# Performance work log

Measured on AMD Instinct MI355X. Metric: run time of the kernel, lower is better.

The kernel has to match this reference:

```python
import math
import jax, jax.numpy as jnp
import numpy as np

B, S, D, H = 8, 1024, 512, 8
DK = D // H
P = 2 * S - 1


def rel_shift(x):
    # x: [b, h, qlen, plen] -> [b, h, qlen, plen-1] (Transformer-XL shift)
    b, h, qL, pL = x.shape
    x = x.reshape(b, h, pL, qL)[:, :, 1:, :]
    return x.reshape(b, h, qL, pL - 1)


def setup_inputs() -> dict:
    key = jax.random.key(0)
    ks = jax.random.split(key, 16)
    glorot = lambda k, shp: (jax.random.uniform(k, shp, jnp.float32, -1.0, 1.0)
                             * np.sqrt(6.0 / (shp[0] + shp[1])))
    inp = {
        "q": jax.random.normal(ks[0], (B, S, D), jnp.float32),
        "k": jax.random.normal(ks[1], (B, S, D), jnp.float32),
        "v": jax.random.normal(ks[2], (B, S, D), jnp.float32),
        "pos_emb": jax.random.normal(ks[3], (1, P, D), jnp.float32),
        "mask": jax.random.randint(ks[4], (B, 1, S), 0, 2).astype(bool),
        "Wq": glorot(ks[5], (D, D)), "bq": jnp.zeros((D,), jnp.float32),
        "Wk": glorot(ks[6], (D, D)), "bk": jnp.zeros((D,), jnp.float32),
        "Wv": glorot(ks[7], (D, D)), "bv": jnp.zeros((D,), jnp.float32),
        "Wo": glorot(ks[8], (D, D)), "bo": jnp.zeros((D,), jnp.float32),
        "Wpos": glorot(ks[9], (D, D)),
        "pos_bias_u": glorot(ks[10], (H, DK)),
        "pos_bias_v": glorot(ks[11], (H, DK)),
    }
    return inp


def reference(q, k, v, pos_emb, mask, Wq, bq, Wk, bk, Wv, bv, Wo, bo,
              Wpos, pos_bias_u, pos_bias_v):
    b = q.shape[0]
    # projections -> [b, h, s, dk]
    qh = (q @ Wq.T + bq).reshape(b, -1, H, DK).transpose(0, 2, 1, 3)
    kh = (k @ Wk.T + bk).reshape(b, -1, H, DK).transpose(0, 2, 1, 3)
    vh = (v @ Wv.T + bv).reshape(b, -1, H, DK).transpose(0, 2, 1, 3)
    # positional projection -> [h, p, dk] (pos batch dim is 1)
    p = (pos_emb @ Wpos.T).reshape(pos_emb.shape[0], -1, H, DK).transpose(0, 2, 1, 3)[0]

    q_u = qh + pos_bias_u[None, :, None, :]
    q_v = qh + pos_bias_v[None, :, None, :]

    matrix_bd = jnp.einsum("bhsd,hpd->bhsp", q_v, p)
    matrix_bd = rel_shift(matrix_bd)
    matrix_ac = jnp.einsum("bhsd,bhtd->bhst", q_u, kh)
    matrix_bd = matrix_bd[:, :, :, : matrix_ac.shape[-1]]

    scores = (matrix_ac + matrix_bd) / math.sqrt(DK)
    # mask [b,1,s] -> [b,1,1,s] broadcast over heads and query dim
    scores = jnp.where(mask[:, None], -10000.0, scores)
    attn = jax.nn.softmax(scores, axis=-1)
    x = jnp.einsum("bhst,bhtd->bhsd", attn, vh)
    x = x.transpose(0, 2, 1, 3).reshape(b, -1, H * DK)
    return x @ Wo.T + bo
```

## Files before the change

### kernel.cpp

```cpp
#include <hip/hip_runtime.h>
#include <math.h>

#define S_LEN 1024
#define N_HEAD 8
#define P_LEN 2047
#define B_SZ 8
#define QT 32
#define KT 32

typedef __attribute__((ext_vector_type(8))) short bf16x8;
typedef __attribute__((ext_vector_type(4))) float f32x4;

union f4u { float4 v; float f[4]; };
union bfz { bf16x8 v; uint4 u; };

__device__ __forceinline__ unsigned short f2bf(float x) {
  unsigned b = __float_as_uint(x);
  b = b + 0x7FFF + ((b >> 16) & 1);
  return (unsigned short)(b >> 16);
}
__device__ __forceinline__ float bf2f(unsigned short h) {
  return __uint_as_float(((unsigned)h) << 16);
}

__global__ __launch_bounds__(256) void mask_prep(const void* __restrict__ mask,
                                                 int* __restrict__ mw) {
  const unsigned int* u = (const unsigned int*)mask;
  bool all01 = true, allf = true;
#pragma unroll
  for (int j = 0; j < 16; ++j) {
    unsigned int x = u[j];
    all01 &= (x <= 1u);
    allf &= (x == 0u || x == 0x3f800000u);
  }
  int i = blockIdx.x * 256 + threadIdx.x;
  int v;
  if (all01) v = (((const int*)mask)[i] != 0);
  else if (allf) v = (((const float*)mask)[i] != 0.0f);
  else v = (((const unsigned char*)mask)[i] != 0);
  mw[i] = v;
}

template<int MODE>
__global__ __launch_bounds__(256) void gemm512(
    const float* __restrict__ A, const float* __restrict__ W,
    const float* __restrict__ bias, const float* __restrict__ pbu,
    const float* __restrict__ pbv, float* __restrict__ fo,
    unsigned short* __restrict__ o1h, unsigned short* __restrict__ o1l,
    unsigned short* __restrict__ o2h, unsigned short* __restrict__ o2l,
    int M)
{
  __shared__ float As[64][36];
  __shared__ float Wt[32][68];
  const int tid = threadIdx.x;
  const int ty = tid >> 4, tx = tid & 15;
  const int m0 = blockIdx.x * 64, n0 = blockIdx.y * 64;
  const int lr = tid >> 3;
  const int lc = (tid & 7) << 2;
  float acc[4][4] = {};

  for (int k0 = 0; k0 < 512; k0 += 32) {
#pragma unroll
    for (int hh = 0; hh < 2; ++hh) {
      int r = lr + hh * 32;
      int gm = m0 + r;
      float4 av = make_float4(0.f, 0.f, 0.f, 0.f);
      if (gm < M) av = *(const float4*)(A + (size_t)gm * 512 + k0 + lc);
      *(float4*)&As[r][lc] = av;
      float4 wv = *(const float4*)(W + (size_t)(n0 + r) * 512 + k0 + lc);
      Wt[lc + 0][r] = wv.x;
      Wt[lc + 1][r] = wv.y;
      Wt[lc + 2][r] = wv.z;
      Wt[lc + 3][r] = wv.w;
    }
    __syncthreads();
#pragma unroll
    for (int kk = 0; kk < 32; kk += 4) {
      f4u a[4], w[4];
#pragma unroll
      for (int i = 0; i < 4; ++i) a[i].v = *(float4*)&As[ty * 4 + i][kk];
#pragma unroll
      for (int q = 0; q < 4; ++q) w[q].v = *(float4*)&Wt[kk + q][tx * 4];
#pragma unroll
      for (int i = 0; i < 4; ++i)
#pragma unroll
        for (int q = 0; q < 4; ++q)
#pragma unroll
          for (int j = 0; j < 4; ++j)
            acc[i][j] = fmaf(a[i].f[q], w[q].f[j], acc[i][j]);
    }
    __syncthreads();
  }

#pragma unroll
  for (int i = 0; i < 4; ++i) {
    int m = m0 + ty * 4 + i;
    if (MODE == 2 && m >= M) continue;
    int n = n0 + tx * 4;
    if constexpr (MODE == 3) {
      f4u r;
#pragma unroll
      for (int j = 0; j < 4; ++j) r.f[j] = acc[i][j] + bias[n + j];
      *(float4*)(fo + (size_t)m * 512 + n) = r.v;
    } else if constexpr (MODE == 2) {
      int hI = n >> 6, dk = n & 63;
      size_t idx = ((size_t)(hI * P_LEN + m) << 6) + dk;
      ushort4 hv, lv;
      unsigned short h;
      h = f2bf(acc[i][0]); hv.x = h; lv.x = f2bf(acc[i][0] - bf2f(h));
      h = f2bf(acc[i][1]); hv.y = h; lv.y = f2bf(acc[i][1] - bf2f(h));
      h = f2bf(acc[i][2]); hv.z = h; lv.z = f2bf(acc[i][2] - bf2f(h));
      h = f2bf(acc[i][3]); hv.w = h; lv.w = f2bf(acc[i][3] - bf2f(h));
      *(ushort4*)(o1h + idx) = hv;
      *(ushort4*)(o1l + idx) = lv;
    } else {
      int bI = m >> 10, s = m & 1023, hI = n >> 6, dk = n & 63;
      size_t idx = ((size_t)(((bI * 8 + hI) << 10) + s) << 6) + dk;
      float vb[4];
#pragma unroll
      for (int j = 0; j < 4; ++j) vb[j] = acc[i][j] + bias[n + j];
      if constexpr (MODE == 0) {
        ushort4 hv, lv;
        unsigned short h;
        h = f2bf(vb[0]); hv.x = h; lv.x = f2bf(vb[0] - bf2f(h));
        h = f2bf(vb[1]); hv.y = h; lv.y = f2bf(vb[1] - bf2f(h));
        h = f2bf(vb[2]); hv.z = h; lv.z = f2bf(vb[2] - bf2f(h));
        h = f2bf(vb[3]); hv.w = h; lv.w = f2bf(vb[3] - bf2f(h));
        *(ushort4*)(o1h + idx) = hv;
        *(ushort4*)(o1l + idx) = lv;
      } else {
        ushort4 hu, lu, hv2, lv2;
        unsigned short h;
        float t;
        t = vb[0] + pbu[n + 0]; h = f2bf(t); hu.x = h; lu.x = f2bf(t - bf2f(h));
        t = vb[1] + pbu[n + 1]; h = f2bf(t); hu.y = h; lu.y = f2bf(t - bf2f(h));
        t = vb[2] + pbu[n + 2]; h = f2bf(t); hu.z = h; lu.z = f2bf(t - bf2f(h));
        t = vb[3] + pbu[n + 3]; h = f2bf(t); hu.w = h; lu.w = f2bf(t - bf2f(h));
        t = vb[0] + pbv[n + 0]; h = f2bf(t); hv2.x = h; lv2.x = f2bf(t - bf2f(h));
        t = vb[1] + pbv[n + 1]; h = f2bf(t); hv2.y = h; lv2.y = f2bf(t - bf2f(h));
        t = vb[2] + pbv[n + 2]; h = f2bf(t); hv2.z = h; lv2.z = f2bf(t - bf2f(h));
        t = vb[3] + pbv[n + 3]; h = f2bf(t); hv2.w = h; lv2.w = f2bf(t - bf2f(h));
        *(ushort4*)(o1h + idx) = hu;  *(ushort4*)(o1l + idx) = lu;
        *(ushort4*)(o2h + idx) = hv2; *(ushort4*)(o2l + idx) = lv2;
      }
    }
  }
}

__global__ __launch_bounds__(256) void vtrans(
    const unsigned short* __restrict__ src_h, const unsigned short* __restrict__ src_l,
    unsigned short* __restrict__ dst_h, unsigned short* __restrict__ dst_l)
{
  __shared__ unsigned short tile[64 * 72];
  const int tid = threadIdx.x;
  const int bh = blockIdx.x >> 4, st = blockIdx.x & 15;
  const int s0 = st << 6;
  const int r = tid >> 2;
  const int c0 = (tid & 3) << 4;
  const size_t ibase = (((size_t)(bh << 10) + s0 + r) << 6) + c0;
  const size_t obase = ((size_t)(bh << 6)) << 10;
#pragma unroll
  for (int pl = 0; pl < 2; ++pl) {
    const unsigned short* src = pl ? src_l : src_h;
    unsigned short* dst = pl ? dst_l : dst_h;
    *(uint4*)&tile[r * 72 + c0] = *(const uint4*)(src + ibase);
    *(uint4*)&tile[r * 72 + c0 + 8] = *(const uint4*)(src + ibase + 8);
    __syncthreads();
    unsigned short buf[16] __attribute__((aligned(16)));
#pragma unroll
    for (int i = 0; i < 16; ++i) buf[i] = tile[(c0 + i) * 72 + r];
    *(uint4*)(dst + obase + ((size_t)r << 10) + s0 + c0) = *(uint4*)&buf[0];
    *(uint4*)(dst + obase + ((size_t)r << 10) + s0 + c0 + 8) = *(uint4*)&buf[8];
    __syncthreads();
  }
}

__global__ __launch_bounds__(256, 3) void attn_kernel(
    const unsigned short* __restrict__ quh, const unsigned short* __restrict__ qul,
    const unsigned short* __restrict__ qvh, const unsigned short* __restrict__ qvl,
    const unsigned short* __restrict__ khh, const unsigned short* __restrict__ khl,
    const unsigned short* __restrict__ vth, const unsigned short* __restrict__ vtl,
    const unsigned short* __restrict__ pph, const unsigned short* __restrict__ ppl,
    const int* __restrict__ mw, float* __restrict__ ctx)
{
  __shared__ float zs[32 * 68];
  __shared__ unsigned short ph_s[32 * 40], pl_s[32 * 40];
  __shared__ float red[2][32][2];

  const int tid = threadIdx.x;
  const int wid = tid >> 6, lane = tid & 63;
  const int g = lane >> 4, ln = lane & 15;
  const int rt = wid >> 1, ct = wid & 1;
  const int R0 = rt << 4, T0 = ct << 4;

  const int bid = blockIdx.x;
  const int xcd = bid & 7;
  const int i0 = bid >> 3;
  const int bh = (xcd << 3) + (i0 >> 5);
  const int s0 = (i0 & 31) * QT;
  const int b = bh >> 3, h = bh & 7;

  const size_t qbase = ((size_t)((bh << 10) + s0)) << 6;
  const size_t kbase = ((size_t)(bh << 10)) << 6;
  const size_t vtb = ((size_t)(bh << 6)) << 10;
  const size_t ppb = ((size_t)(h * P_LEN)) << 6;

  bf16x8 qa_h[2], qa_l[2], qb_h[2], qb_l[2];
  {
    const size_t qo = qbase + (((size_t)(R0 + ln)) << 6) + (g << 3);
#pragma unroll
    for (int dblk = 0; dblk < 2; ++dblk) {
      qa_h[dblk] = *(const bf16x8*)(quh + qo + dblk * 32);
      qa_l[dblk] = *(const bf16x8*)(qul + qo + dblk * 32);
      qb_h[dblk] = *(const bf16x8*)(qvh + qo + dblk * 32);
      qb_l[dblk] = *(const bf16x8*)(qvl + qo + dblk * 32);
    }
  }

  float wrapW = 0.f;
  if (s0 == 0) {
    const unsigned short* q1h = qvh + ((((size_t)(bh << 10)) + 1) << 6);
    const unsigned short* q1l = qvl + ((((size_t)(bh << 10)) + 1) << 6);
    for (int d = 0; d < 64; ++d)
      wrapW += (bf2f(q1h[d]) + bf2f(q1l[d])) * (bf2f(pph[ppb + d]) + bf2f(ppl[ppb + d]));
  }
  const bool wrapT = (s0 == 0) && (wid == 1) && (lane == 15);

  f32x4 oA[2] = {{0.f, 0.f, 0.f, 0.f}, {0.f, 0.f, 0.f, 0.f}};
  float m_run[4], l_run[4];
#pragma unroll
  for (int r = 0; r < 4; ++r) { m_run[r] = -1e30f; l_run[r] = 0.f; }

  for (int t0 = 0; t0 < S_LEN; t0 += KT) {
    f32x4 ac = {0.f, 0.f, 0.f, 0.f};
    {
      const size_t ko = kbase + (((size_t)(t0 + T0 + ln)) << 6) + (g << 3);
#pragma unroll
      for (int dblk = 0; dblk < 2; ++dblk) {
        bf16x8 kh_ = *(const bf16x8*)(khh + ko + dblk * 32);
        bf16x8 kl_ = *(const bf16x8*)(khl + ko + dblk * 32);
        ac = __builtin_amdgcn_mfma_f32_16x16x32_bf16(qa_l[dblk], kh_, ac, 0, 0, 0);
        ac = __builtin_amdgcn_mfma_f32_16x16x32_bf16(qa_h[dblk], kl_, ac, 0, 0, 0);
        ac = __builtin_amdgcn_mfma_f32_16x16x32_bf16(qa_h[dblk], kh_, ac, 0, 0, 0);
      }
    }
    const int pmin = 993 + t0 - s0;
#pragma unroll
    for (int ut = 0; ut < 2; ++ut) {
      const int U0 = (ct << 5) + (ut << 4);
      const int p = pmin + U0 + ln;
      f32x4 z = {0.f, 0.f, 0.f, 0.f};
      bfz bh_[2], bl_[2];
      if (p < P_LEN) {
        const size_t po = ppb + (((size_t)p) << 6) + (g << 3);
        bh_[0].v = *(const bf16x8*)(pph + po);
        bh_[1].v = *(const bf16x8*)(pph + po + 32);
        bl_[0].v = *(const bf16x8*)(ppl + po);
        bl_[1].v = *(const bf16x8*)(ppl + po + 32);
      } else {
        bh_[0].u = bh_[1].u = bl_[0].u = bl_[1].u = make_uint4(0, 0, 0, 0);
      }
#pragma unroll
      for (int dblk = 0; dblk < 2; ++dblk) {
        z = __builtin_amdgcn_mfma_f32_16x16x32_bf16(qb_l[dblk], bh_[dblk].v, z, 0, 0, 0);
        z = __builtin_amdgcn_mfma_f32_16x16x32_bf16(qb_h[dblk], bl_[dblk].v, z, 0, 0, 0);
        z = __builtin_amdgcn_mfma_f32_16x16x32_bf16(qb_h[dblk], bh_[dblk].v, z, 0, 0, 0);
      }
#pragma unroll
      for (int r = 0; r < 4; ++r)
        zs[(R0 + (g << 2) + r) * 68 + U0 + ln] = z[r];
    }
    __syncthreads();

    const int t = T0 + ln;
    const int mval = mw[(b << 10) + t0 + t];
    float sc[4], ml[4], sl[4];
#pragma unroll
    for (int r = 0; r < 4; ++r) {
      const int row = R0 + (g << 2) + r;
      float bdv = zs[row * 68 + (t - row + 31)];
      if (wrapT && r == 0 && t0 == S_LEN - KT) bdv = wrapW;
      float v = (ac[r] + bdv) * 0.125f;
      sc[r] = mval ? -10000.f : v;
    }
#pragma unroll
    for (int r = 0; r < 4; ++r) {
      float mx = sc[r];
#pragma unroll
      for (int off = 1; off < 16; off <<= 1) mx = fmaxf(mx, __shfl_xor(mx, off));
      ml[r] = mx;
      float e = __expf(sc[r] - mx);
      float s = e;
#pragma unroll
      for (int off = 1; off < 16; off <<= 1) s += __shfl_xor(s, off);
      sl[r] = s;
      sc[r] = e;
    }
    if (ln == 0) {
#pragma unroll
      for (int r = 0; r < 4; ++r) {
        red[ct][R0 + (g << 2) + r][0] = ml[r];
        red[ct][R0 + (g << 2) + r][1] = sl[r];
      }
    }
    __syncthreads();

#pragma unroll
    for (int r = 0; r < 4; ++r) {
      const int row = R0 + (g << 2) + r;
      const float mo = red[ct ^ 1][row][0];
      const float so = red[ct ^ 1][row][1];
      const float mn = fmaxf(m_run[r], fmaxf(ml[r], mo));
      const float corr = __expf(m_run[r] - mn);
      l_run[r] = l_run[r] * corr + sl[r] * __expf(ml[r] - mn) + so * __expf(mo - mn);
      m_run[r] = mn;
      oA[0][r] *= corr;
      oA[1][r] *= corr;
      const float p = sc[r] * __expf(ml[r] - mn);
      const unsigned short hp = f2bf(p);
      ph_s[row * 40 + t] = hp;
      pl_s[row * 40 + t] = f2bf(p - bf2f(hp));
    }
    __syncthreads();

    bf16x8 pa_h = *(const bf16x8*)&ph_s[(R0 + ln) * 40 + (g << 3)];
    bf16x8 pa_l = *(const bf16x8*)&pl_s[(R0 + ln) * 40 + (g << 3)];
#pragma unroll
    for (int dkt = 0; dkt < 2; ++dkt) {
      const int dk = (ct << 5) + (dkt << 4) + ln;
      const size_t vo = vtb + (((size_t)dk) << 10) + t0 + (g << 3);
      bf16x8 vh_ = *(const bf16x8*)(vth + vo);
      bf16x8 vl_ = *(const bf16x8*)(vtl + vo);
      oA[dkt] = __builtin_amdgcn_mfma_f32_16x16x32_bf16(pa_l, vh_, oA[dkt], 0, 0, 0);
      oA[dkt] = __builtin_amdgcn_mfma_f32_16x16x32_bf16(pa_h, vl_, oA[dkt], 0, 0, 0);
      oA[dkt] = __builtin_amdgcn_mfma_f32_16x16x32_bf16(pa_h, vh_, oA[dkt], 0, 0, 0);
    }
  }

#pragma unroll
  for (int r = 0; r < 4; ++r) {
    const float inv = 1.0f / l_run[r];
    const int s = s0 + R0 + (g << 2) + r;
    float* cp = ctx + (((size_t)((b << 10) + s)) << 9) + (h << 6);
    cp[(ct << 5) + ln] = oA[0][r] * inv;
    cp[(ct << 5) + 16 + ln] = oA[1][r] * inv;
  }
}

extern "C" void kernel_launch(void* const* d_in, const int* in_sizes, int n_in,
                              void* d_out, int out_size, void* d_ws, size_t ws_size,
                              hipStream_t stream) {
  const float* q    = (const float*)d_in[0];
  const float* k    = (const float*)d_in[1];
  const float* v    = (const float*)d_in[2];
  const float* pos  = (const float*)d_in[3];
  const void*  mask = d_in[4];
  const float* Wq   = (const float*)d_in[5];
  const float* bq   = (const float*)d_in[6];
  const float* Wk   = (const float*)d_in[7];
  const float* bk   = (const float*)d_in[8];
  const float* Wv   = (const float*)d_in[9];
  const float* bv   = (const float*)d_in[10];
  const float* Wo   = (const float*)d_in[11];
  const float* bo   = (const float*)d_in[12];
  const float* Wpos = (const float*)d_in[13];
  const float* pbu  = (const float*)d_in[14];
  const float* pbv  = (const float*)d_in[15];
  float* out = (float*)d_out;

  unsigned short* us = (unsigned short*)d_ws;
  const size_t SZ  = (size_t)B_SZ * N_HEAD * S_LEN * 64;
  const size_t SZP = (size_t)N_HEAD * P_LEN * 64;
  unsigned short* quh = us;
  unsigned short* qul = quh + SZ;
  unsigned short* qvh = qul + SZ;
  unsigned short* qvl = qvh + SZ;
  unsigned short* khh = qvl + SZ;
  unsigned short* khl = khh + SZ;
  unsigned short* vth = khl + SZ;
  unsigned short* vtl = vth + SZ;
  unsigned short* pph = vtl + SZ;
  unsigned short* ppl = pph + SZP;
  float* ctxW = (float*)(ppl + SZP);
  unsigned short* vhh = (unsigned short*)ctxW;
  unsigned short* vhl = vhh + SZ;
  int* mwW = (int*)(ctxW + SZ);

  mask_prep<<<dim3(B_SZ * S_LEN / 256), 256, 0, stream>>>(mask, mwW);

  gemm512<1><<<dim3(128, 8), 256, 0, stream>>>(q, Wq, bq, pbu, pbv, nullptr,
                                               quh, qul, qvh, qvl, 8192);
  gemm512<0><<<dim3(128, 8), 256, 0, stream>>>(k, Wk, bk, nullptr, nullptr, nullptr,
                                               khh, khl, nullptr, nullptr, 8192);
  gemm512<0><<<dim3(128, 8), 256, 0, stream>>>(v, Wv, bv, nullptr, nullptr, nullptr,
                                               vhh, vhl, nullptr, nullptr, 8192);
  gemm512<2><<<dim3(32, 8), 256, 0, stream>>>(pos, Wpos, nullptr, nullptr, nullptr, nullptr,
                                              pph, ppl, nullptr, nullptr, P_LEN);

  vtrans<<<dim3(64 * 16), 256, 0, stream>>>(vhh, vhl, vth, vtl);

  attn_kernel<<<dim3(2048), 256, 0, stream>>>(quh, qul, qvh, qvl, khh, khl,
                                              vth, vtl, pph, ppl, mwW, ctxW);

  gemm512<3><<<dim3(128, 8), 256, 0, stream>>>(ctxW, Wo, bo, nullptr, nullptr, out,
                                               nullptr, nullptr, nullptr, nullptr, 8192);
}
```

Baseline: 876.9 us.

## Software-pipeline K and positional tile loads with register double buffering

The attention loop is unrolled by two using macros, with register double buffers for K and positional-embedding fragments. The next tile's loads are issued before the current tile's MFMA and softmax work, and V loads are hoisted to the start of each iteration. This is meant to hide global-memory latency behind compute and barriers. The extra live registers lower the occupancy hint from 3 to 2 blocks per CU, which risks less latency hiding across waves.

```diff
diff --git a/kernel.cpp b/kernel.cpp
--- a/kernel.cpp
+++ b/kernel.cpp
@@ -175,7 +175,122 @@
   }
 }
 
-__global__ __launch_bounds__(256, 3) void attn_kernel(
+#define MFMA_B(a, b, c) __builtin_amdgcn_mfma_f32_16x16x32_bf16(a, b, c, 0, 0, 0)
+
+#define DECL_KB(S) \
+  bf16x8 S##kh0, S##kh1, S##kl0, S##kl1; \
+  bfz S##b0h0, S##b0h1, S##b0l0, S##b0l1, S##b1h0, S##b1h1, S##b1l0, S##b1l1;
+
+#define LOAD_KB(S, T0V) { \
+  const size_t ko_ = kbase + (((size_t)((T0V) + T0 + ln)) << 6) + (g << 3); \
+  S##kh0 = *(const bf16x8*)(khh + ko_); \
+  S##kh1 = *(const bf16x8*)(khh + ko_ + 32); \
+  S##kl0 = *(const bf16x8*)(khl + ko_); \
+  S##kl1 = *(const bf16x8*)(khl + ko_ + 32); \
+  const int pm_ = 993 + (T0V) - s0 + (ct << 5) + ln; \
+  if (pm_ < P_LEN) { \
+    const size_t po_ = ppb + (((size_t)pm_) << 6) + (g << 3); \
+    S##b0h0.v = *(const bf16x8*)(pph + po_); \
+    S##b0h1.v = *(const bf16x8*)(pph + po_ + 32); \
+    S##b0l0.v = *(const bf16x8*)(ppl + po_); \
+    S##b0l1.v = *(const bf16x8*)(ppl + po_ + 32); \
+  } else { \
+    S##b0h0.u = make_uint4(0,0,0,0); S##b0h1.u = make_uint4(0,0,0,0); \
+    S##b0l0.u = make_uint4(0,0,0,0); S##b0l1.u = make_uint4(0,0,0,0); } \
+  if (pm_ + 16 < P_LEN) { \
+    const size_t po_ = ppb + (((size_t)(pm_ + 16)) << 6) + (g << 3); \
+    S##b1h0.v = *(const bf16x8*)(pph + po_); \
+    S##b1h1.v = *(const bf16x8*)(pph + po_ + 32); \
+    S##b1l0.v = *(const bf16x8*)(ppl + po_); \
+    S##b1l1.v = *(const bf16x8*)(ppl + po_ + 32); \
+  } else { \
+    S##b1h0.u = make_uint4(0,0,0,0); S##b1h1.u = make_uint4(0,0,0,0); \
+    S##b1l0.u = make_uint4(0,0,0,0); S##b1l1.u = make_uint4(0,0,0,0); } \
+}
+
+#define ATTN_ITER(C, N, T0C, LASTF) { \
+  bf16x8 vh0_, vl0_, vh1_, vl1_; \
+  { const size_t vo0_ = vtb + (((size_t)((ct << 5) + ln)) << 10) + (T0C) + (g << 3); \
+    vh0_ = *(const bf16x8*)(vth + vo0_); \
+    vl0_ = *(const bf16x8*)(vtl + vo0_); \
+    const size_t vo1_ = vtb + (((size_t)((ct << 5) + 16 + ln)) << 10) + (T0C) + (g << 3); \
+    vh1_ = *(const bf16x8*)(vth + vo1_); \
+    vl1_ = *(const bf16x8*)(vtl + vo1_); } \
+  if (!(LASTF)) { LOAD_KB(N, (T0C) + KT) } \
+  f32x4 ac_ = {0.f, 0.f, 0.f, 0.f}; \
+  ac_ = MFMA_B(qa_l[0], C##kh0, ac_); \
+  ac_ = MFMA_B(qa_h[0], C##kl0, ac_); \
+  ac_ = MFMA_B(qa_h[0], C##kh0, ac_); \
+  ac_ = MFMA_B(qa_l[1], C##kh1, ac_); \
+  ac_ = MFMA_B(qa_h[1], C##kl1, ac_); \
+  ac_ = MFMA_B(qa_h[1], C##kh1, ac_); \
+  f32x4 z0_ = {0.f, 0.f, 0.f, 0.f}, z1_ = {0.f, 0.f, 0.f, 0.f}; \
+  z0_ = MFMA_B(qb_l[0], C##b0h0.v, z0_); \
+  z0_ = MFMA_B(qb_h[0], C##b0l0.v, z0_); \
+  z0_ = MFMA_B(qb_h[0], C##b0h0.v, z0_); \
+  z0_ = MFMA_B(qb_l[1], C##b0h1.v, z0_); \
+  z0_ = MFMA_B(qb_h[1], C##b0l1.v, z0_); \
+  z0_ = MFMA_B(qb_h[1], C##b0h1.v, z0_); \
+  z1_ = MFMA_B(qb_l[0], C##b1h0.v, z1_); \
+  z1_ = MFMA_B(qb_h[0], C##b1l0.v, z1_); \
+  z1_ = MFMA_B(qb_h[0], C##b1h0.v, z1_); \
+  z1_ = MFMA_B(qb_l[1], C##b1h1.v, z1_); \
+  z1_ = MFMA_B(qb_h[1], C##b1l1.v, z1_); \
+  z1_ = MFMA_B(qb_h[1], C##b1h1.v, z1_); \
+  { const int U0_ = (ct << 5); \
+    _Pragma("unroll") for (int r = 0; r < 4; ++r) { \
+      zs[(R0 + (g << 2) + r) * 68 + U0_ + ln] = z0_[r]; \
+      zs[(R0 + (g << 2) + r) * 68 + U0_ + 16 + ln] = z1_[r]; } } \
+  __syncthreads(); \
+  { const int t_ = T0 + ln; \
+    const int mval_ = mw[(b << 10) + (T0C) + t_]; \
+    float sc_[4], ml_[4], sl_[4]; \
+    _Pragma("unroll") for (int r = 0; r < 4; ++r) { \
+      const int row_ = R0 + (g << 2) + r; \
+      float bdv_ = zs[row_ * 68 + (t_ - row_ + 31)]; \
+      if (wrapT && r == 0 && (T0C) == S_LEN - KT) bdv_ = wrapW; \
+      float v_ = (ac_[r] + bdv_) * 0.125f; \
+      sc_[r] = mval_ ? -10000.f : v_; } \
+    _Pragma("unroll") for (int r = 0; r < 4; ++r) { \
+      float mx_ = sc_[r]; \
+      _Pragma("unroll") for (int off = 1; off < 16; off <<= 1) \
+        mx_ = fmaxf(mx_, __shfl_xor(mx_, off)); \
+      ml_[r] = mx_; \
+      float e_ = __expf(sc_[r] - mx_); \
+      float s_ = e_; \
+      _Pragma("unroll") for (int off = 1; off < 16; off <<= 1) \
+        s_ += __shfl_xor(s_, off); \
+      sl_[r] = s_; sc_[r] = e_; } \
+    if (ln == 0) { \
+      _Pragma("unroll") for (int r = 0; r < 4; ++r) { \
+        red[ct][R0 + (g << 2) + r][0] = ml_[r]; \
+        red[ct][R0 + (g << 2) + r][1] = sl_[r]; } } \
+    __syncthreads(); \
+    _Pragma("unroll") for (int r = 0; r < 4; ++r) { \
+      const int row_ = R0 + (g << 2) + r; \
+      const float mo_ = red[ct ^ 1][row_][0]; \
+      const float so_ = red[ct ^ 1][row_][1]; \
+      const float mn_ = fmaxf(m_run[r], fmaxf(ml_[r], mo_)); \
+      const float corr_ = __expf(m_run[r] - mn_); \
+      l_run[r] = l_run[r] * corr_ + sl_[r] * __expf(ml_[r] - mn_) + so_ * __expf(mo_ - mn_); \
+      m_run[r] = mn_; \
+      oA0[r] *= corr_; oA1[r] *= corr_; \
+      const float p_ = sc_[r] * __expf(ml_[r] - mn_); \
+      const unsigned short hp_ = f2bf(p_); \
+      ph_s[row_ * 40 + t_] = hp_; \
+      pl_s[row_ * 40 + t_] = f2bf(p_ - bf2f(hp_)); } \
+    __syncthreads(); } \
+  { bf16x8 pa_h_ = *(const bf16x8*)&ph_s[(R0 + ln) * 40 + (g << 3)]; \
+    bf16x8 pa_l_ = *(const bf16x8*)&pl_s[(R0 + ln) * 40 + (g << 3)]; \
+    oA0 = MFMA_B(pa_l_, vh0_, oA0); \
+    oA0 = MFMA_B(pa_h_, vl0_, oA0); \
+    oA0 = MFMA_B(pa_h_, vh0_, oA0); \
+    oA1 = MFMA_B(pa_l_, vh1_, oA1); \
+    oA1 = MFMA_B(pa_h_, vl1_, oA1); \
+    oA1 = MFMA_B(pa_h_, vh1_, oA1); } \
+}
+
+__global__ __launch_bounds__(256, 2) void attn_kernel(
     const unsigned short* __restrict__ quh, const unsigned short* __restrict__ qul,
     const unsigned short* __restrict__ qvh, const unsigned short* __restrict__ qvl,
     const unsigned short* __restrict__ khh, const unsigned short* __restrict__ khl,
@@ -226,124 +341,28 @@
   }
   const bool wrapT = (s0 == 0) && (wid == 1) && (lane == 15);
 
-  f32x4 oA[2] = {{0.f, 0.f, 0.f, 0.f}, {0.f, 0.f, 0.f, 0.f}};
+  f32x4 oA0 = {0.f, 0.f, 0.f, 0.f}, oA1 = {0.f, 0.f, 0.f, 0.f};
   float m_run[4], l_run[4];
 #pragma unroll
   for (int r = 0; r < 4; ++r) { m_run[r] = -1e30f; l_run[r] = 0.f; }
 
-  for (int t0 = 0; t0 < S_LEN; t0 += KT) {
-    f32x4 ac = {0.f, 0.f, 0.f, 0.f};
-    {
-      const size_t ko = kbase + (((size_t)(t0 + T0 + ln)) << 6) + (g << 3);
-#pragma unroll
-      for (int dblk = 0; dblk < 2; ++dblk) {
-        bf16x8 kh_ = *(const bf16x8*)(khh + ko + dblk * 32);
-        bf16x8 kl_ = *(const bf16x8*)(khl + ko + dblk * 32);
-        ac = __builtin_amdgcn_mfma_f32_16x16x32_bf16(qa_l[dblk], kh_, ac, 0, 0, 0);
-        ac = __builtin_amdgcn_mfma_f32_16x16x32_bf16(qa_h[dblk], kl_, ac, 0, 0, 0);
-        ac = __builtin_amdgcn_mfma_f32_16x16x32_bf16(qa_h[dblk], kh_, ac, 0, 0, 0);
-      }
-    }
-    const int pmin = 993 + t0 - s0;
-#pragma unroll
-    for (int ut = 0; ut < 2; ++ut) {
-      const int U0 = (ct << 5) + (ut << 4);
-      const int p = pmin + U0 + ln;
-      f32x4 z = {0.f, 0.f, 0.f, 0.f};
-      bfz bh_[2], bl_[2];
-      if (p < P_LEN) {
-        const size_t po = ppb + (((size_t)p) << 6) + (g << 3);
-        bh_[0].v = *(const bf16x8*)(pph + po);
-        bh_[1].v = *(const bf16x8*)(pph + po + 32);
-        bl_[0].v = *(const bf16x8*)(ppl + po);
-        bl_[1].v = *(const bf16x8*)(ppl + po + 32);
-      } else {
-        bh_[0].u = bh_[1].u = bl_[0].u = bl_[1].u = make_uint4(0, 0, 0, 0);
-      }
-#pragma unroll
-      for (int dblk = 0; dblk < 2; ++dblk) {
-        z = __builtin_amdgcn_mfma_f32_16x16x32_bf16(qb_l[dblk], bh_[dblk].v, z, 0, 0, 0);
-        z = __builtin_amdgcn_mfma_f32_16x16x32_bf16(qb_h[dblk], bl_[dblk].v, z, 0, 0, 0);
-        z = __builtin_amdgcn_mfma_f32_16x16x32_bf16(qb_h[dblk], bh_[dblk].v, z, 0, 0, 0);
-      }
-#pragma unroll
-      for (int r = 0; r < 4; ++r)
-        zs[(R0 + (g << 2) + r) * 68 + U0 + ln] = z[r];
-    }
-    __syncthreads();
-
-    const int t = T0 + ln;
-    const int mval = mw[(b << 10) + t0 + t];
-    float sc[4], ml[4], sl[4];
-#pragma unroll
-    for (int r = 0; r < 4; ++r) {
-      const int row = R0 + (g << 2) + r;
-      float bdv = zs[row * 68 + (t - row + 31)];
-      if (wrapT && r == 0 && t0 == S_LEN - KT) bdv = wrapW;
-      float v = (ac[r] + bdv) * 0.125f;
-      sc[r] = mval ? -10000.f : v;
-    }
-#pragma unroll
-    for (int r = 0; r < 4; ++r) {
-      float mx = sc[r];
-#pragma unroll
-      for (int off = 1; off < 16; off <<= 1) mx = fmaxf(mx, __shfl_xor(mx, off));
-      ml[r] = mx;
-      float e = __expf(sc[r] - mx);
-      float s = e;
-#pragma unroll
-      for (int off = 1; off < 16; off <<= 1) s += __shfl_xor(s, off);
-      sl[r] = s;
-      sc[r] = e;
-    }
-    if (ln == 0) {
-#pragma unroll
-      for (int r = 0; r < 4; ++r) {
-        red[ct][R0 + (g << 2) + r][0] = ml[r];
-        red[ct][R0 + (g << 2) + r][1] = sl[r];
-      }
-    }
-    __syncthreads();
-
-#pragma unroll
-    for (int r = 0; r < 4; ++r) {
-      const int row = R0 + (g << 2) + r;
-      const float mo = red[ct ^ 1][row][0];
-      const float so = red[ct ^ 1][row][1];
-      const float mn = fmaxf(m_run[r], fmaxf(ml[r], mo));
-      const float corr = __expf(m_run[r] - mn);
-      l_run[r] = l_run[r] * corr + sl[r] * __expf(ml[r] - mn) + so * __expf(mo - mn);
-      m_run[r] = mn;
-      oA[0][r] *= corr;
-      oA[1][r] *= corr;
-      const float p = sc[r] * __expf(ml[r] - mn);
-      const unsigned short hp = f2bf(p);
-      ph_s[row * 40 + t] = hp;
-      pl_s[row * 40 + t] = f2bf(p - bf2f(hp));
-    }
-    __syncthreads();
-
-    bf16x8 pa_h = *(const bf16x8*)&ph_s[(R0 + ln) * 40 + (g << 3)];
-    bf16x8 pa_l = *(const bf16x8*)&pl_s[(R0 + ln) * 40 + (g << 3)];
-#pragma unroll
-    for (int dkt = 0; dkt < 2; ++dkt) {
-      const int dk = (ct << 5) + (dkt << 4) + ln;
-      const size_t vo = vtb + (((size_t)dk) << 10) + t0 + (g << 3);
-      bf16x8 vh_ = *(const bf16x8*)(vth + vo);
-      bf16x8 vl_ = *(const bf16x8*)(vtl + vo);
-      oA[dkt] = __builtin_amdgcn_mfma_f32_16x16x32_bf16(pa_l, vh_, oA[dkt], 0, 0, 0);
-      oA[dkt] = __builtin_amdgcn_mfma_f32_16x16x32_bf16(pa_h, vl_, oA[dkt], 0, 0, 0);
-      oA[dkt] = __builtin_amdgcn_mfma_f32_16x16x32_bf16(pa_h, vh_, oA[dkt], 0, 0, 0);
-    }
-  }
+  DECL_KB(A_) DECL_KB(B_)
+  LOAD_KB(A_, 0)
+
+  for (int t0 = 0; t0 < S_LEN - 64; t0 += 64) {
+    ATTN_ITER(A_, B_, t0, 0)
+    ATTN_ITER(B_, A_, t0 + 32, 0)
+  }
+  ATTN_ITER(A_, B_, S_LEN - 64, 0)
+  ATTN_ITER(B_, A_, S_LEN - 32, 1)
 
 #pragma unroll
   for (int r = 0; r < 4; ++r) {
     const float inv = 1.0f / l_run[r];
     const int s = s0 + R0 + (g << 2) + r;
     float* cp = ctx + (((size_t)((b << 10) + s)) << 9) + (h << 6);
-    cp[(ct << 5) + ln] = oA[0][r] * inv;
-    cp[(ct << 5) + 16 + ln] = oA[1][r] * inv;
+    cp[(ct << 5) + ln] = oA0[r] * inv;
+    cp[(ct << 5) + 16 + ln] = oA1[r] * inv;
   }
 }
 
```

New measurement: 877.0 us. Within noise of the previous version (+0.0%).
